# Kernel optimization log

Measured on AMD Instinct MI355X. Metric: run time of the kernel, lower is better.

The kernel has to match this reference:

```python
import math
import jax, jax.numpy as jnp
import numpy as np

B, H, D, N, M = 4, 8, 64, 8192, 256
EPS = 1e-6


def sample_orthogonal_random_vectors(num_rows, num_cols, seed=0):
    """Faithful port of FavorAttention.sample_orthogonal_random_vectors."""
    rng = np.random.default_rng(seed)
    num_blocks = math.ceil(num_rows / num_cols)
    unstructured = rng.standard_normal((num_blocks, num_cols, num_cols)).astype(np.float32)
    norm = np.linalg.norm(unstructured, axis=-1).reshape(-1, 1)
    q, _ = np.linalg.qr(unstructured)                 # reduced QR per block
    q = np.transpose(q, (0, 2, 1)).reshape(-1, num_cols)
    q = q[:num_rows, :] * norm[:num_rows, :]
    return jnp.asarray(q, dtype=jnp.float32)


def setup_inputs() -> dict:
    key = jax.random.key(0)
    kq, kk, kv = jax.random.split(key, 3)
    return {
        "query": jax.random.normal(kq, (B, H, D, N), dtype=jnp.float32),
        "key": jax.random.normal(kk, (B, H, D, N), dtype=jnp.float32),
        "value": jax.random.normal(kv, (B, H, D, N), dtype=jnp.float32),
        "projection_matrix": sample_orthogonal_random_vectors(M, D),
    }


def randomized_kernel(x, proj, is_query, eps=EPS):
    """FAVOR+ positive softmax features. x: [B,H,D,N] -> phi: [B,H,M,N]."""
    d = x.shape[2]
    data_normalizer = d ** -0.25
    ratio = proj.shape[0] ** -0.5
    # projected: [B,H,M,N]
    u = jnp.einsum('md,bhdn->bhmn', proj, x) * data_normalizer
    # ||x||^2 / (2*sqrt(d)) per token: [B,H,1,N]
    diag = jnp.sum(x * x, axis=2, keepdims=True) * (data_normalizer ** 2) * 0.5
    if is_query:
        stab = jnp.max(u, axis=2, keepdims=True)            # per-token max over features
    else:
        stab = jnp.max(u, axis=(2, 3), keepdims=True)       # global max per (b,h)
    return ratio * (jnp.exp(u - diag - stab) + eps)


def reference(query, key, value, projection_matrix):
    q_phi = randomized_kernel(query, projection_matrix, is_query=True)    # [B,H,M,N]
    k_phi = randomized_kernel(key, projection_matrix, is_query=False)     # [B,H,M,N]
    # kv = key @ value^T over sequence: [B,H,M,D]
    kv = jnp.einsum('bhmn,bhdn->bhmd', k_phi, value)
    key_norm = jnp.sum(k_phi, axis=3)                                     # [B,H,M]
    out = jnp.einsum('bhmn,bhmd->bhnd', q_phi, kv)                        # [B,H,N,D]
    out_norm = jnp.einsum('bhmn,bhm->bhn', q_phi, key_norm)[..., None]    # [B,H,N,1]
    out = out / out_norm
    return jnp.swapaxes(out, 2, 3)                                        # [B,H,D,N]


if __name__ == '__main__':
    o = reference(**setup_inputs())
    print(o.shape, o.dtype)
```

## Files before the change

kernel.cpp:

```cpp
#include <hip/hip_runtime.h>


typedef short s16x8 __attribute__((ext_vector_type(8)));
typedef float f32x4 __attribute__((ext_vector_type(4)));

#define Dv 64
#define Nv 8192
#define Mv 256
#define BHv 32
#define SPL 16
#define NSPL (Nv / SPL)
#define NCH (NSPL / 64)

#define DNRM 0.3535533905932738f
#define EPSV 1e-6f

#define OFF_SGM 0
#define OFF_SVP (OFF_SGM + BHv * SPL * 4)
#define OFF_KNP (OFF_SVP + BHv * SPL * 64)
#define OFF_KNF (OFF_KNP + BHv * SPL * Mv)
#define OFF_KVP (OFF_KNF + BHv * Mv)
#define OFF_KVT (OFF_KVP + BHv * SPL * Mv * Dv)

__device__ __forceinline__ unsigned short f2b(float x) {
    return __builtin_bit_cast(unsigned short, (__bf16)x);
}

__device__ __forceinline__ s16x8 load_pfrag(const float* __restrict__ proj, int m,
                                            int kc, int q) {
    const float* p = proj + m * 64 + kc * 32 + q * 8;
    s16x8 r;
#pragma unroll
    for (int j = 0; j < 8; ++j) r[j] = (short)f2b(p[j]);
    return r;
}

__global__ __launch_bounds__(256, 2) void favor_kv(const float* __restrict__ key,
                                                   const float* __restrict__ value,
                                                   const float* __restrict__ proj,
                                                   float* __restrict__ ws) {
    __shared__ __align__(16) unsigned short KT[64][72];
    __shared__ __align__(16) unsigned short VL[64][72];
    __shared__ __align__(16) unsigned short PH[256][40];
    __shared__ __align__(16) float dred[16][64];
    __shared__ __align__(16) float dgl[64];
    const int tid = threadIdx.x;
    const int w = tid >> 6, l = tid & 63, c = l & 15, q = l >> 4;
    const int g = tid >> 4, cs = tid & 15;
    const int s = blockIdx.x, bh = blockIdx.y;
    const float* kp = key + (size_t)bh * Dv * Nv;
    const float* vp = value + (size_t)bh * Dv * Nv;

    s16x8 P[4][2];
#pragma unroll
    for (int mt = 0; mt < 4; ++mt)
#pragma unroll
        for (int kc = 0; kc < 2; ++kc)
            P[mt][kc] = load_pfrag(proj, (4 * w + mt) * 16 + c, kc, q);

    f32x4 kva[4][4];
#pragma unroll
    for (int mt = 0; mt < 4; ++mt)
#pragma unroll
        for (int dt = 0; dt < 4; ++dt) kva[mt][dt] = (f32x4){0.f, 0.f, 0.f, 0.f};
    float kn[4] = {0.f, 0.f, 0.f, 0.f};
    float sv[4] = {0.f, 0.f, 0.f, 0.f};
    float mx = -3.0e38f;

    for (int ch = 0; ch < NCH; ++ch) {
        const int n0 = s * NSPL + ch * 64;
        if (ch) __syncthreads();
        {
            float4 kk[4], vv[4];
#pragma unroll
            for (int di = 0; di < 4; ++di) {
                kk[di] = *(const float4*)&kp[(4 * g + di) * Nv + n0 + 4 * cs];
                vv[di] = *(const float4*)&vp[(4 * g + di) * Nv + n0 + 4 * cs];
            }
#pragma unroll
            for (int j = 0; j < 4; ++j) {
                const float k0 = ((const float*)&kk[0])[j];
                const float k1 = ((const float*)&kk[1])[j];
                const float k2 = ((const float*)&kk[2])[j];
                const float k3 = ((const float*)&kk[3])[j];
                *(short4*)&KT[4 * cs + j][4 * g] =
                    make_short4((short)f2b(k0), (short)f2b(k1), (short)f2b(k2),
                                (short)f2b(k3));
                dred[g][4 * cs + j] = (k0 * k0 + k1 * k1) + (k2 * k2 + k3 * k3);
            }
#pragma unroll
            for (int di = 0; di < 4; ++di) {
                *(short4*)&VL[4 * g + di][4 * cs] = make_short4(
                    (short)f2b(vv[di].x), (short)f2b(vv[di].y),
                    (short)f2b(vv[di].z), (short)f2b(vv[di].w));
                sv[di] += (vv[di].x + vv[di].y) + (vv[di].z + vv[di].w);
            }
        }
        __syncthreads();
        if (tid < 64) {
            float ds = 0.f;
#pragma unroll
            for (int gg = 0; gg < 16; ++gg) ds += dred[gg][tid];
            dgl[tid] = ds * 0.0625f;
        }
        __syncthreads();
#pragma unroll
        for (int h = 0; h < 2; ++h) {
            f32x4 u[4][2];
#pragma unroll
            for (int nt2 = 0; nt2 < 2; ++nt2) {
                const int nt = 2 * h + nt2;
                const s16x8 a0 = *(const s16x8*)&KT[nt * 16 + c][q * 8];
                const s16x8 a1 = *(const s16x8*)&KT[nt * 16 + c][32 + q * 8];
#pragma unroll
                for (int mt = 0; mt < 4; ++mt) {
                    f32x4 t = {0.f, 0.f, 0.f, 0.f};
                    t = __builtin_amdgcn_mfma_f32_16x16x32_bf16(a0, P[mt][0], t, 0, 0, 0);
                    t = __builtin_amdgcn_mfma_f32_16x16x32_bf16(a1, P[mt][1], t, 0, 0, 0);
                    u[mt][nt2] = t;
                }
            }
            float cm = -3.0e38f;
#pragma unroll
            for (int mt = 0; mt < 4; ++mt)
#pragma unroll
                for (int nt2 = 0; nt2 < 2; ++nt2)
                    cm = fmaxf(cm, fmaxf(fmaxf(u[mt][nt2][0], u[mt][nt2][1]),
                                         fmaxf(u[mt][nt2][2], u[mt][nt2][3])));
            cm *= DNRM;
#pragma unroll
            for (int off = 1; off < 64; off <<= 1)
                cm = fmaxf(cm, __shfl_xor(cm, off, 64));
            if (cm > mx) {
                const float al = __expf(mx - cm);
#pragma unroll
                for (int mt = 0; mt < 4; ++mt) {
#pragma unroll
                    for (int dt = 0; dt < 4; ++dt) kva[mt][dt] *= al;
                    kn[mt] *= al;
                }
                mx = cm;
            }
#pragma unroll
            for (int nt2 = 0; nt2 < 2; ++nt2) {
                const int nt = 2 * h + nt2;
                const float4 dg = *(const float4*)&dgl[nt * 16 + q * 4];
#pragma unroll
                for (int mt = 0; mt < 4; ++mt) {
                    const float e0 = __expf(u[mt][nt2][0] * DNRM - dg.x - mx);
                    const float e1 = __expf(u[mt][nt2][1] * DNRM - dg.y - mx);
                    const float e2 = __expf(u[mt][nt2][2] * DNRM - dg.z - mx);
                    const float e3 = __expf(u[mt][nt2][3] * DNRM - dg.w - mx);
                    kn[mt] += (e0 + e1) + (e2 + e3);
                    *(short4*)&PH[(4 * w + mt) * 16 + c][nt2 * 16 + q * 4] =
                        make_short4((short)f2b(e0), (short)f2b(e1),
                                    (short)f2b(e2), (short)f2b(e3));
                }
            }
            s16x8 bf[4];
#pragma unroll
            for (int dt = 0; dt < 4; ++dt)
                bf[dt] = *(const s16x8*)&VL[dt * 16 + c][h * 32 + q * 8];
#pragma unroll
            for (int mt = 0; mt < 4; ++mt) {
                const s16x8 a = *(const s16x8*)&PH[(4 * w + mt) * 16 + c][q * 8];
#pragma unroll
                for (int dt = 0; dt < 4; ++dt)
                    kva[mt][dt] = __builtin_amdgcn_mfma_f32_16x16x32_bf16(
                        a, bf[dt], kva[mt][dt], 0, 0, 0);
            }
        }
    }
    float* kvp = ws + OFF_KVP + (size_t)(bh * SPL + s) * Mv * Dv;
#pragma unroll
    for (int mt = 0; mt < 4; ++mt) {
        const int mrow = (4 * w + mt) * 16 + 4 * q;
#pragma unroll
        for (int dt = 0; dt < 4; ++dt) {
            const int dcol = dt * 16 + c;
#pragma unroll
            for (int r = 0; r < 4; ++r)
                kvp[(size_t)(mrow + r) * Dv + dcol] = kva[mt][dt][r];
        }
    }
#pragma unroll
    for (int mt = 0; mt < 4; ++mt) {
        kn[mt] += __shfl_xor(kn[mt], 16, 64);
        kn[mt] += __shfl_xor(kn[mt], 32, 64);
    }
    if (q == 0) {
        float* knp = ws + OFF_KNP + (bh * SPL + s) * Mv;
#pragma unroll
        for (int mt = 0; mt < 4; ++mt) knp[(4 * w + mt) * 16 + c] = kn[mt];
    }
    if (l == 0) ws[OFF_SGM + (bh * SPL + s) * 4 + w] = mx;
    __syncthreads();
    float* sp = &dred[0][0];
#pragma unroll
    for (int di = 0; di < 4; ++di) sp[(4 * g + di) * 16 + cs] = sv[di];
    __syncthreads();
    if (tid < 64) {
        float t2 = 0.f;
#pragma unroll
        for (int j = 0; j < 16; ++j) t2 += sp[tid * 16 + j];
        ws[OFF_SVP + (bh * SPL + s) * 64 + tid] = t2;
    }
}

__global__ __launch_bounds__(256) void favor_kvred(float* __restrict__ ws) {
    __shared__ float sgl[64];
    __shared__ float alph[SPL];
    __shared__ float svl[64];
    __shared__ float Gs;
    const int t = threadIdx.x, f = blockIdx.x, bh = blockIdx.y;
    const int flat = f * 1024 + t * 4;
    const int m = flat >> 6, d0 = flat & 63;
    const int wgrp = f >> 2;
    if (t < 64) {
        const float v = ws[OFF_SGM + bh * 64 + t];
        sgl[t] = v;
        float gm = v;
#pragma unroll
        for (int off = 1; off < 64; off <<= 1)
            gm = fmaxf(gm, __shfl_xor(gm, off, 64));
        if (t == 0) Gs = gm;
    } else if (t < 128) {
        const int d = t - 64;
        float x = 0.f;
#pragma unroll
        for (int s2 = 0; s2 < SPL; ++s2)
            x += ws[OFF_SVP + (bh * SPL + s2) * 64 + d];
        svl[d] = x;
    }
    __syncthreads();
    if (t < SPL) alph[t] = __expf(sgl[t * 4 + wgrp] - Gs);
    __syncthreads();
    float4 acc = make_float4(0.f, 0.f, 0.f, 0.f);
    for (int s2 = 0; s2 < SPL; ++s2) {
        const float a = alph[s2];
        const float4 v =
            *(const float4*)&ws[OFF_KVP + ((size_t)(bh * SPL + s2) << 14) + flat];
        acc.x += a * v.x; acc.y += a * v.y; acc.z += a * v.z; acc.w += a * v.w;
    }
    acc.x += EPSV * svl[d0 + 0];
    acc.y += EPSV * svl[d0 + 1];
    acc.z += EPSV * svl[d0 + 2];
    acc.w += EPSV * svl[d0 + 3];
    unsigned short* kvT = (unsigned short*)(ws + OFF_KVT);
    kvT[(bh * 64 + d0 + 0) * 256 + m] = f2b(acc.x);
    kvT[(bh * 64 + d0 + 1) * 256 + m] = f2b(acc.y);
    kvT[(bh * 64 + d0 + 2) * 256 + m] = f2b(acc.z);
    kvT[(bh * 64 + d0 + 3) * 256 + m] = f2b(acc.w);
    if (t < 16) {
        const int mm = f * 16 + t;
        float kk = 0.f;
        for (int s2 = 0; s2 < SPL; ++s2)
            kk += alph[s2] * ws[OFF_KNP + (bh * SPL + s2) * Mv + mm];
        ws[OFF_KNF + bh * Mv + mm] = kk + EPSV * (float)Nv;
    }
}

__global__ __launch_bounds__(256, 2) void favor_out(const float* __restrict__ query,
                                                    const float* __restrict__ proj,
                                                    const float* __restrict__ ws,
                                                    float* __restrict__ out) {
    __shared__ __align__(16) unsigned short PHT[64][264];
    __shared__ float npart[4][64];
    __shared__ float knl[256];
    __shared__ float cw[4][64];
    __shared__ float stabl[64];
    __shared__ float dql[64];
    unsigned short (*QT)[72] = (unsigned short (*)[72]) & PHT[0][0];
    float (*dred)[64] = (float (*)[64])((char*)&PHT[0][0] + 9216);
    const int tid = threadIdx.x;
    const int w = tid >> 6, l = tid & 63, c = l & 15, q = l >> 4;
    const int g = tid >> 4, cs = tid & 15;
    const int nb = blockIdx.x, bh = blockIdx.y;
    const int n0 = nb * 64;
    const float* qp = query + (size_t)bh * Dv * Nv;
    const unsigned short* kvT =
        (const unsigned short*)(ws + OFF_KVT) + (size_t)bh * 64 * 256;

    {
        float4 qq[4];
#pragma unroll
        for (int di = 0; di < 4; ++di)
            qq[di] = *(const float4*)&qp[(4 * g + di) * Nv + n0 + 4 * cs];
#pragma unroll
        for (int j = 0; j < 4; ++j) {
            const float v0 = ((const float*)&qq[0])[j];
            const float v1 = ((const float*)&qq[1])[j];
            const float v2 = ((const float*)&qq[2])[j];
            const float v3 = ((const float*)&qq[3])[j];
            *(short4*)&QT[4 * cs + j][4 * g] =
                make_short4((short)f2b(v0), (short)f2b(v1), (short)f2b(v2),
                            (short)f2b(v3));
            dred[g][4 * cs + j] = (v0 * v0 + v1 * v1) + (v2 * v2 + v3 * v3);
        }
    }
    knl[tid] = ws[OFF_KNF + bh * Mv + tid];

    s16x8 P[4][2];
#pragma unroll
    for (int mt = 0; mt < 4; ++mt)
#pragma unroll
        for (int kc = 0; kc < 2; ++kc)
            P[mt][kc] = load_pfrag(proj, (4 * w + mt) * 16 + c, kc, q);
    __syncthreads();

    f32x4 u[4][4];
#pragma unroll
    for (int mt = 0; mt < 4; ++mt)
#pragma unroll
        for (int nt = 0; nt < 4; ++nt) u[mt][nt] = (f32x4){0.f, 0.f, 0.f, 0.f};
#pragma unroll
    for (int nt = 0; nt < 4; ++nt) {
        const s16x8 b0 = *(const s16x8*)&QT[nt * 16 + c][q * 8];
        const s16x8 b1 = *(const s16x8*)&QT[nt * 16 + c][32 + q * 8];
#pragma unroll
        for (int mt = 0; mt < 4; ++mt) {
            u[mt][nt] =
                __builtin_amdgcn_mfma_f32_16x16x32_bf16(P[mt][0], b0, u[mt][nt], 0, 0, 0);
            u[mt][nt] =
                __builtin_amdgcn_mfma_f32_16x16x32_bf16(P[mt][1], b1, u[mt][nt], 0, 0, 0);
        }
    }
#pragma unroll
    for (int nt = 0; nt < 4; ++nt) {
        float vm = -3.4e38f;
#pragma unroll
        for (int mt = 0; mt < 4; ++mt)
            vm = fmaxf(vm, fmaxf(fmaxf(u[mt][nt][0], u[mt][nt][1]),
                                 fmaxf(u[mt][nt][2], u[mt][nt][3])));
        vm = fmaxf(vm, __shfl_xor(vm, 16, 64));
        vm = fmaxf(vm, __shfl_xor(vm, 32, 64));
        if (q == 0) cw[w][nt * 16 + c] = vm;
    }
    __syncthreads();
    if (tid < 64) {
        stabl[tid] =
            fmaxf(fmaxf(cw[0][tid], cw[1][tid]), fmaxf(cw[2][tid], cw[3][tid]));
        float dsum = 0.f;
#pragma unroll
        for (int gg = 0; gg < 16; ++gg) dsum += dred[gg][tid];
        dql[tid] = dsum * 0.0625f;
    }
    __syncthreads();
#pragma unroll
    for (int nt = 0; nt < 4; ++nt) {
        const float sr = stabl[nt * 16 + c];
        const float dq = dql[nt * 16 + c];
        float np = 0.f;
#pragma unroll
        for (int mt = 0; mt < 4; ++mt) {
            const float e0 = __expf((u[mt][nt][0] - sr) * DNRM - dq) + EPSV;
            const float e1 = __expf((u[mt][nt][1] - sr) * DNRM - dq) + EPSV;
            const float e2 = __expf((u[mt][nt][2] - sr) * DNRM - dq) + EPSV;
            const float e3 = __expf((u[mt][nt][3] - sr) * DNRM - dq) + EPSV;
            const int mb = (4 * w + mt) * 16 + 4 * q;
            np += e0 * knl[mb] + e1 * knl[mb + 1] + e2 * knl[mb + 2] +
                  e3 * knl[mb + 3];
            *(short4*)&PHT[nt * 16 + c][mb] = make_short4(
                (short)f2b(e0), (short)f2b(e1), (short)f2b(e2), (short)f2b(e3));
        }
        np += __shfl_xor(np, 16, 64);
        np += __shfl_xor(np, 32, 64);
        if (q == 0) npart[w][nt * 16 + c] = np;
    }
    __syncthreads();
    f32x4 acc[4];
#pragma unroll
    for (int dt = 0; dt < 4; ++dt) acc[dt] = (f32x4){0.f, 0.f, 0.f, 0.f};
#pragma unroll
    for (int kc = 0; kc < 8; ++kc) {
        const s16x8 a = *(const s16x8*)&PHT[w * 16 + c][kc * 32 + q * 8];
#pragma unroll
        for (int dt = 0; dt < 4; ++dt) {
            const s16x8 b =
                *(const s16x8*)&kvT[(size_t)(dt * 16 + c) * 256 + kc * 32 + q * 8];
            acc[dt] = __builtin_amdgcn_mfma_f32_16x16x32_bf16(a, b, acc[dt], 0, 0, 0);
        }
    }
    __syncthreads();
    float* ot = (float*)&PHT[0][0];
    float rn[4];
#pragma unroll
    for (int r = 0; r < 4; ++r) {
        const int nl = w * 16 + 4 * q + r;
        rn[r] = 1.0f / ((npart[0][nl] + npart[1][nl]) +
                        (npart[2][nl] + npart[3][nl]));
    }
#pragma unroll
    for (int dt = 0; dt < 4; ++dt)
#pragma unroll
        for (int r = 0; r < 4; ++r)
            ot[(dt * 16 + c) * 68 + (w * 16 + 4 * q + r)] = acc[dt][r] * rn[r];
    __syncthreads();
    float* op = out + (size_t)bh * Dv * Nv;
    {
        const int d = tid >> 2, ng = (tid & 3) * 16;
#pragma unroll
        for (int i = 0; i < 4; ++i) {
            const float4 v = *(const float4*)&ot[d * 68 + ng + i * 4];
            *(float4*)&op[d * Nv + n0 + ng + i * 4] = v;
        }
    }
}

extern "C" void kernel_launch(void* const* d_in, const int* in_sizes, int n_in,
                              void* d_out, int out_size, void* d_ws, size_t ws_size,
                              hipStream_t stream) {
    const float* q = (const float*)d_in[0];
    const float* k = (const float*)d_in[1];
    const float* v = (const float*)d_in[2];
    const float* proj = (const float*)d_in[3];
    float* ws = (float*)d_ws;
    float* out = (float*)d_out;

    favor_kv<<<dim3(SPL, 32), 256, 0, stream>>>(k, v, proj, ws);
    favor_kvred<<<dim3(16, 32), 256, 0, stream>>>(ws);
    favor_out<<<dim3(Nv / 64, 32), 256, 0, stream>>>(q, proj, ws, out);
}
```

Baseline: 321.6 us.

## Use fixed exp stabilizer and atomic accumulation for key-value partials

Replaces the per-chunk online max rescaling in the key-feature pass with a fixed constant stabilizer. The true global max is still tracked and applied as one rescale factor in the reduction kernel. Split partials for kv, key-norm and value sums are now accumulated with atomics into zeroed buffers instead of being written per split and reduced later, so the reduction kernel shrinks to a single scale-and-transpose pass. This removes shuffle reductions, branches and rescales from the hot loop, but adds a memset, float-atomic contention and nondeterminism, and risks exp overflow or underflow if projected values fall far from the fixed constant.

```diff
diff --git a/kernel.cpp b/kernel.cpp
--- a/kernel.cpp
+++ b/kernel.cpp
@@ -14,13 +14,15 @@
 
 #define DNRM 0.3535533905932738f
 #define EPSV 1e-6f
-
-#define OFF_SGM 0
-#define OFF_SVP (OFF_SGM + BHv * SPL * 4)
-#define OFF_KNP (OFF_SVP + BHv * SPL * 64)
-#define OFF_KNF (OFF_KNP + BHv * SPL * Mv)
-#define OFF_KVP (OFF_KNF + BHv * Mv)
-#define OFF_KVT (OFF_KVP + BHv * SPL * Mv * Dv)
+#define KSTAB 15.0f
+
+#define OFF_KVA 0
+#define OFF_KNA (OFF_KVA + BHv * Mv * Dv)
+#define OFF_SVA (OFF_KNA + BHv * Mv)
+#define OFF_SGM (OFF_SVA + BHv * Dv)
+#define OFF_KNF (OFF_SGM + BHv * 64)
+#define OFF_KVT (OFF_KNF + BHv * Mv)
+#define ZERO_FLOATS (OFF_SVA + BHv * Dv)
 
 __device__ __forceinline__ unsigned short f2b(float x) {
     return __builtin_bit_cast(unsigned short, (__bf16)x);
@@ -65,7 +67,7 @@
         for (int dt = 0; dt < 4; ++dt) kva[mt][dt] = (f32x4){0.f, 0.f, 0.f, 0.f};
     float kn[4] = {0.f, 0.f, 0.f, 0.f};
     float sv[4] = {0.f, 0.f, 0.f, 0.f};
-    float mx = -3.0e38f;
+    float tmax = -3.0e38f;
 
     for (int ch = 0; ch < NCH; ++ch) {
         const int n0 = s * NSPL + ch * 64;
@@ -106,51 +108,22 @@
         __syncthreads();
 #pragma unroll
         for (int h = 0; h < 2; ++h) {
-            f32x4 u[4][2];
 #pragma unroll
             for (int nt2 = 0; nt2 < 2; ++nt2) {
                 const int nt = 2 * h + nt2;
                 const s16x8 a0 = *(const s16x8*)&KT[nt * 16 + c][q * 8];
                 const s16x8 a1 = *(const s16x8*)&KT[nt * 16 + c][32 + q * 8];
+                const float4 dg = *(const float4*)&dgl[nt * 16 + q * 4];
 #pragma unroll
                 for (int mt = 0; mt < 4; ++mt) {
-                    f32x4 t = {0.f, 0.f, 0.f, 0.f};
-                    t = __builtin_amdgcn_mfma_f32_16x16x32_bf16(a0, P[mt][0], t, 0, 0, 0);
-                    t = __builtin_amdgcn_mfma_f32_16x16x32_bf16(a1, P[mt][1], t, 0, 0, 0);
-                    u[mt][nt2] = t;
-                }
-            }
-            float cm = -3.0e38f;
-#pragma unroll
-            for (int mt = 0; mt < 4; ++mt)
-#pragma unroll
-                for (int nt2 = 0; nt2 < 2; ++nt2)
-                    cm = fmaxf(cm, fmaxf(fmaxf(u[mt][nt2][0], u[mt][nt2][1]),
-                                         fmaxf(u[mt][nt2][2], u[mt][nt2][3])));
-            cm *= DNRM;
-#pragma unroll
-            for (int off = 1; off < 64; off <<= 1)
-                cm = fmaxf(cm, __shfl_xor(cm, off, 64));
-            if (cm > mx) {
-                const float al = __expf(mx - cm);
-#pragma unroll
-                for (int mt = 0; mt < 4; ++mt) {
-#pragma unroll
-                    for (int dt = 0; dt < 4; ++dt) kva[mt][dt] *= al;
-                    kn[mt] *= al;
-                }
-                mx = cm;
-            }
-#pragma unroll
-            for (int nt2 = 0; nt2 < 2; ++nt2) {
-                const int nt = 2 * h + nt2;
-                const float4 dg = *(const float4*)&dgl[nt * 16 + q * 4];
-#pragma unroll
-                for (int mt = 0; mt < 4; ++mt) {
-                    const float e0 = __expf(u[mt][nt2][0] * DNRM - dg.x - mx);
-                    const float e1 = __expf(u[mt][nt2][1] * DNRM - dg.y - mx);
-                    const float e2 = __expf(u[mt][nt2][2] * DNRM - dg.z - mx);
-                    const float e3 = __expf(u[mt][nt2][3] * DNRM - dg.w - mx);
+                    f32x4 u = {0.f, 0.f, 0.f, 0.f};
+                    u = __builtin_amdgcn_mfma_f32_16x16x32_bf16(a0, P[mt][0], u, 0, 0, 0);
+                    u = __builtin_amdgcn_mfma_f32_16x16x32_bf16(a1, P[mt][1], u, 0, 0, 0);
+                    tmax = fmaxf(tmax, fmaxf(fmaxf(u[0], u[1]), fmaxf(u[2], u[3])));
+                    const float e0 = __expf(u[0] * DNRM - dg.x - KSTAB);
+                    const float e1 = __expf(u[1] * DNRM - dg.y - KSTAB);
+                    const float e2 = __expf(u[2] * DNRM - dg.z - KSTAB);
+                    const float e3 = __expf(u[3] * DNRM - dg.w - KSTAB);
                     kn[mt] += (e0 + e1) + (e2 + e3);
                     *(short4*)&PH[(4 * w + mt) * 16 + c][nt2 * 16 + q * 4] =
                         make_short4((short)f2b(e0), (short)f2b(e1),
@@ -171,7 +144,11 @@
             }
         }
     }
-    float* kvp = ws + OFF_KVP + (size_t)(bh * SPL + s) * Mv * Dv;
+#pragma unroll
+    for (int off = 1; off < 64; off <<= 1)
+        tmax = fmaxf(tmax, __shfl_xor(tmax, off, 64));
+    if (l == 0) ws[OFF_SGM + bh * 64 + s * 4 + w] = tmax * DNRM;
+    float* kvp = ws + OFF_KVA + (size_t)bh * Mv * Dv;
 #pragma unroll
     for (int mt = 0; mt < 4; ++mt) {
         const int mrow = (4 * w + mt) * 16 + 4 * q;
@@ -180,7 +157,7 @@
             const int dcol = dt * 16 + c;
 #pragma unroll
             for (int r = 0; r < 4; ++r)
-                kvp[(size_t)(mrow + r) * Dv + dcol] = kva[mt][dt][r];
+                atomicAdd(&kvp[(size_t)(mrow + r) * Dv + dcol], kva[mt][dt][r]);
         }
     }
 #pragma unroll
@@ -189,11 +166,10 @@
         kn[mt] += __shfl_xor(kn[mt], 32, 64);
     }
     if (q == 0) {
-        float* knp = ws + OFF_KNP + (bh * SPL + s) * Mv;
-#pragma unroll
-        for (int mt = 0; mt < 4; ++mt) knp[(4 * w + mt) * 16 + c] = kn[mt];
-    }
-    if (l == 0) ws[OFF_SGM + (bh * SPL + s) * 4 + w] = mx;
+#pragma unroll
+        for (int mt = 0; mt < 4; ++mt)
+            atomicAdd(&ws[OFF_KNA + bh * Mv + (4 * w + mt) * 16 + c], kn[mt]);
+    }
     __syncthreads();
     float* sp = &dred[0][0];
 #pragma unroll
@@ -203,60 +179,44 @@
         float t2 = 0.f;
 #pragma unroll
         for (int j = 0; j < 16; ++j) t2 += sp[tid * 16 + j];
-        ws[OFF_SVP + (bh * SPL + s) * 64 + tid] = t2;
+        atomicAdd(&ws[OFF_SVA + bh * 64 + tid], t2);
     }
 }
 
 __global__ __launch_bounds__(256) void favor_kvred(float* __restrict__ ws) {
-    __shared__ float sgl[64];
-    __shared__ float alph[SPL];
-    __shared__ float svl[64];
-    __shared__ float Gs;
+    __shared__ float sAl;
     const int t = threadIdx.x, f = blockIdx.x, bh = blockIdx.y;
-    const int flat = f * 1024 + t * 4;
+    if (t < 64) {
+        float v = ws[OFF_SGM + bh * 64 + t];
+#pragma unroll
+        for (int off = 1; off < 64; off <<= 1)
+            v = fmaxf(v, __shfl_xor(v, off, 64));
+        if (t == 0) sAl = __expf(KSTAB - v);
+    }
+    __syncthreads();
+    const float al = sAl;
+    const int flat = f * 4096 + t * 16;
     const int m = flat >> 6, d0 = flat & 63;
-    const int wgrp = f >> 2;
+    const float* kva = ws + OFF_KVA + (size_t)bh * Mv * Dv;
+    const float* sva = ws + OFF_SVA + bh * 64;
+    unsigned short* kvT =
+        (unsigned short*)(ws + OFF_KVT) + (size_t)bh * 64 * 256;
+    float4 vv[4];
+#pragma unroll
+    for (int i = 0; i < 4; ++i) vv[i] = *(const float4*)&kva[flat + 4 * i];
+#pragma unroll
+    for (int i = 0; i < 4; ++i) {
+#pragma unroll
+        for (int j = 0; j < 4; ++j) {
+            const int d = d0 + 4 * i + j;
+            const float val = ((const float*)&vv[i])[j] * al + EPSV * sva[d];
+            kvT[(size_t)d * 256 + m] = f2b(val);
+        }
+    }
     if (t < 64) {
-        const float v = ws[OFF_SGM + bh * 64 + t];
-        sgl[t] = v;
-        float gm = v;
-#pragma unroll
-        for (int off = 1; off < 64; off <<= 1)
-            gm = fmaxf(gm, __shfl_xor(gm, off, 64));
-        if (t == 0) Gs = gm;
-    } else if (t < 128) {
-        const int d = t - 64;
-        float x = 0.f;
-#pragma unroll
-        for (int s2 = 0; s2 < SPL; ++s2)
-            x += ws[OFF_SVP + (bh * SPL + s2) * 64 + d];
-        svl[d] = x;
-    }
-    __syncthreads();
-    if (t < SPL) alph[t] = __expf(sgl[t * 4 + wgrp] - Gs);
-    __syncthreads();
-    float4 acc = make_float4(0.f, 0.f, 0.f, 0.f);
-    for (int s2 = 0; s2 < SPL; ++s2) {
-        const float a = alph[s2];
-        const float4 v =
-            *(const float4*)&ws[OFF_KVP + ((size_t)(bh * SPL + s2) << 14) + flat];
-        acc.x += a * v.x; acc.y += a * v.y; acc.z += a * v.z; acc.w += a * v.w;
-    }
-    acc.x += EPSV * svl[d0 + 0];
-    acc.y += EPSV * svl[d0 + 1];
-    acc.z += EPSV * svl[d0 + 2];
-    acc.w += EPSV * svl[d0 + 3];
-    unsigned short* kvT = (unsigned short*)(ws + OFF_KVT);
-    kvT[(bh * 64 + d0 + 0) * 256 + m] = f2b(acc.x);
-    kvT[(bh * 64 + d0 + 1) * 256 + m] = f2b(acc.y);
-    kvT[(bh * 64 + d0 + 2) * 256 + m] = f2b(acc.z);
-    kvT[(bh * 64 + d0 + 3) * 256 + m] = f2b(acc.w);
-    if (t < 16) {
-        const int mm = f * 16 + t;
-        float kk = 0.f;
-        for (int s2 = 0; s2 < SPL; ++s2)
-            kk += alph[s2] * ws[OFF_KNP + (bh * SPL + s2) * Mv + mm];
-        ws[OFF_KNF + bh * Mv + mm] = kk + EPSV * (float)Nv;
+        const int mm = f * 64 + t;
+        ws[OFF_KNF + bh * Mv + mm] =
+            ws[OFF_KNA + bh * Mv + mm] * al + EPSV * (float)Nv;
     }
 }
 
@@ -417,7 +377,8 @@
     float* ws = (float*)d_ws;
     float* out = (float*)d_out;
 
+    hipMemsetAsync(ws, 0, (size_t)ZERO_FLOATS * sizeof(float), stream);
     favor_kv<<<dim3(SPL, 32), 256, 0, stream>>>(k, v, proj, ws);
-    favor_kvred<<<dim3(16, 32), 256, 0, stream>>>(ws);
+    favor_kvred<<<dim3(4, 32), 256, 0, stream>>>(ws);
     favor_out<<<dim3(Nv / 64, 32), 256, 0, stream>>>(q, proj, ws, out);
 }
```

After: 332.5 us. 1.03x slower.
